# Performance work log

Measured on AMD Instinct MI355X. Metric: run time of the kernel, lower is better.

## Reference

```python
import jax, jax.numpy as jnp
import numpy as np

NEG_SLOPE = 0.2  # PyG GATv2Conv default

N_NODES = 10000
N_EDGES = 320000
DIM_IN = 128
DIM_H = 32
HEADS = 8
DIM_OUT = 32
HID = DIM_H * HEADS  # 256


def _gatv2(x, src, dst, Wl, Wr, att, bias, heads, ch, n):
    # x: [N, Fin]; src/dst: [E] (self-loops already included)
    xl = (x @ Wl).reshape(n, heads, ch)  # source-side transform
    xr = (x @ Wr).reshape(n, heads, ch)  # target-side transform
    e = jax.nn.leaky_relu(xl[src] + xr[dst], NEG_SLOPE)       # [E, H, C]
    score = jnp.einsum('ehc,hc->eh', e, att)                  # [E, H]
    m = jax.ops.segment_max(score, dst, num_segments=n)        # [N, H]
    ex = jnp.exp(score - m[dst])
    denom = jax.ops.segment_sum(ex, dst, num_segments=n)
    alpha = ex / (denom[dst] + 1e-16)                          # [E, H]
    out = jax.ops.segment_sum(alpha[:, :, None] * xl[src], dst, num_segments=n)
    return out.reshape(n, heads * ch) + bias


def setup_inputs() -> dict:
    key = jax.random.key(0)
    ks = jax.random.split(key, 16)
    x = jax.random.normal(ks[0], (N_NODES, DIM_IN), dtype=jnp.float32)
    edge_index = jax.random.randint(ks[1], (2, N_EDGES), 0, N_NODES, dtype=jnp.int64)

    def glorot(k, shape, fan_in):
        return jax.random.normal(k, shape, dtype=jnp.float32) * (1.0 / np.sqrt(fan_in))

    return {
        'x': x,
        'W1l': glorot(ks[2], (DIM_IN, HID), DIM_IN),
        'W1r': glorot(ks[3], (DIM_IN, HID), DIM_IN),
        'a1': glorot(ks[4], (HEADS, DIM_H), DIM_H),
        'b1': jnp.zeros((HID,), dtype=jnp.float32),
        'W2l': glorot(ks[5], (HID, HID), HID),
        'W2r': glorot(ks[6], (HID, HID), HID),
        'a2': glorot(ks[7], (HEADS, DIM_H), DIM_H),
        'b2': jnp.zeros((HID,), dtype=jnp.float32),
        'W3l': glorot(ks[8], (HID, DIM_OUT), HID),
        'W3r': glorot(ks[9], (HID, DIM_OUT), HID),
        'a3': glorot(ks[10], (1, DIM_OUT), DIM_OUT),
        'b3': jnp.zeros((DIM_OUT,), dtype=jnp.float32),
        'edge_index': edge_index,
    }


def reference(x, W1l, W1r, a1, b1, W2l, W2r, a2, b2, W3l, W3r, a3, b3, edge_index):
    n = x.shape[0]
    loops = jnp.arange(n, dtype=edge_index.dtype)
    src = jnp.concatenate([edge_index[0], loops])
    dst = jnp.concatenate([edge_index[1], loops])

    # eval mode: dropout(p=0.6) is identity
    h = _gatv2(x, src, dst, W1l, W1r, a1, b1, HEADS, DIM_H, n)
    h = jax.nn.relu(h)
    h_res = h
    h = _gatv2(h, src, dst, W2l, W2r, a2, b2, HEADS, DIM_H, n)
    h = h + h_res
    h = _gatv2(h, src, dst, W3l, W3r, a3, b3, 1, DIM_OUT, n)
    return h
```

## Files before the change

### kernel.cpp

```cpp
#include <hip/hip_runtime.h>

#define N_NODES 10000
#define N_EDGES 320000
#define E_TOT   (N_EDGES + N_NODES)
#define HID 256
#define NEG_SLOPE 0.2f
#define SLOTS 192

typedef __attribute__((ext_vector_type(8))) short short8;
typedef __attribute__((ext_vector_type(4))) float float4v;

__device__ int   g_cnt[N_NODES];
__device__ int   g_csr[(size_t)N_NODES * SLOTS];
__device__ __align__(16) float g_xl[(size_t)N_NODES * HID];
__device__ __align__(16) float g_xr[(size_t)N_NODES * HID];
__device__ __align__(16) float g_h1[(size_t)N_NODES * HID];
__device__ __align__(16) unsigned short g_xlb[(size_t)N_NODES * HID];
__device__ __align__(16) unsigned short g_abf[(size_t)N_NODES * 512];
__device__ __align__(16) unsigned short g_bp1a[16 * 8  * 64 * 8];
__device__ __align__(16) unsigned short g_bp2a[16 * 8  * 64 * 8];
__device__ __align__(16) unsigned short g_bp1b[16 * 16 * 64 * 8];
__device__ __align__(16) unsigned short g_bp2b[16 * 16 * 64 * 8];
__device__ __align__(16) unsigned short g_bp1c[2  * 16 * 64 * 8];
__device__ __align__(16) unsigned short g_bp2c[2  * 16 * 64 * 8];

__device__ __forceinline__ unsigned short f2bf(float f) {
    unsigned int u = __float_as_uint(f);
    unsigned int r = (u + 0x7fffu + ((u >> 16) & 1u)) >> 16;
    return (unsigned short)r;
}
__device__ __forceinline__ float bf2f(unsigned short h) {
    return __uint_as_float(((unsigned int)h) << 16);
}
__device__ __forceinline__ unsigned int splitpack(float f) {
    unsigned short hi = f2bf(f);
    unsigned short lo = f2bf(f - bf2f(hi));
    return ((unsigned int)lo << 16) | hi;
}

__device__ __forceinline__ void packB(const float* __restrict__ B,
                                      unsigned short* __restrict__ Bp,
                                      int t, int nkc, int N) {
    int lane = t & 63;
    int kc   = (t >> 6) % nkc;
    int nt   = (t >> 6) / nkc;
    int n = nt * 16 + (lane & 15);
    int kbase = kc * 32 + (lane >> 4) * 8;
    #pragma unroll
    for (int j = 0; j < 8; ++j) {
        int kp = kbase + j;
        int k  = kp >> 1;
        float f = B[(size_t)k * N + n];
        unsigned short hi = f2bf(f);
        Bp[(size_t)t * 8 + j] = (kp & 1) ? f2bf(f - bf2f(hi)) : hi;
    }
}

__global__ __launch_bounds__(256) void k_prep(const float* __restrict__ W1l,
                                              const float* __restrict__ W1r,
                                              const float* __restrict__ W2l,
                                              const float* __restrict__ W2r,
                                              const float* __restrict__ W3l,
                                              const float* __restrict__ W3r,
                                              unsigned short* bp1a, unsigned short* bp2a,
                                              unsigned short* bp1b, unsigned short* bp2b,
                                              unsigned short* bp1c, unsigned short* bp2c,
                                              int* __restrict__ cnt) {
    const int S0 = 16 * 8 * 64;
    const int S1 = 16 * 16 * 64;
    const int S2 = 2 * 16 * 64;
    int t = blockIdx.x * blockDim.x + threadIdx.x;
    if (t < S0) {
        packB(W1l, bp1a, t, 8, 256);
        packB(W1r, bp2a, t, 8, 256);
    } else if (t < S0 + S1) {
        int u = t - S0;
        packB(W2l, bp1b, u, 16, 256);
        packB(W2r, bp2b, u, 16, 256);
    } else if (t < S0 + S1 + S2) {
        int u = t - S0 - S1;
        packB(W3l, bp1c, u, 16, 32);
        packB(W3r, bp2c, u, 16, 32);
    } else {
        int u = t - S0 - S1 - S2;
        if (u < N_NODES) cnt[u] = 0;
    }
}

#define FILL_BLOCKS ((E_TOT + 255) / 256)
__global__ __launch_bounds__(256) void k_fill_gemm1(
    const int* __restrict__ ei,
    int* __restrict__ cnt, int* __restrict__ csr,
    const float4* __restrict__ A4,
    const short8* __restrict__ Bp1, const short8* __restrict__ Bp2,
    unsigned short* __restrict__ C1b,
    float* __restrict__ C2)
{
    if (blockIdx.x < FILL_BLOCKS) {
        int e = blockIdx.x * 256 + threadIdx.x;
        if (e < E_TOT) {
            int src, dst;
            if (e < N_EDGES) { src = ei[e]; dst = ei[N_EDGES + e]; }
            else             { src = dst = e - N_EDGES; }
            int pos = atomicAdd(&cnt[dst], 1);
            if (pos < SLOTS) csr[dst * SLOTS + pos] = src;
        }
        return;
    }
    const int nkc = 8;
    int mt   = blockIdx.x - FILL_BLOCKS;
    int lane = threadIdx.x & 63;
    int wid  = threadIdx.x >> 6;
    int quad = lane >> 4;
    int col  = lane & 15;
    int r0 = mt * 32 + col;       if (r0 >= N_NODES) r0 = N_NODES - 1;
    int r1 = mt * 32 + 16 + col;  if (r1 >= N_NODES) r1 = N_NODES - 1;
    const float4* a0 = A4 + (size_t)r0 * 32 + quad;
    const float4* a1 = A4 + (size_t)r1 * 32 + quad;
    float4v acc[2][4][2];
    #pragma unroll
    for (int s = 0; s < 2; ++s)
        #pragma unroll
        for (int t = 0; t < 4; ++t) { acc[s][t][0] = (float4v)(0.f); acc[s][t][1] = (float4v)(0.f); }
    for (int kc = 0; kc < nkc; ++kc) {
        float4 v0 = a0[kc * 4];
        float4 v1 = a1[kc * 4];
        union { short8 s; unsigned int u[4]; } c0, c1;
        c0.u[0] = splitpack(v0.x); c0.u[1] = splitpack(v0.y);
        c0.u[2] = splitpack(v0.z); c0.u[3] = splitpack(v0.w);
        c1.u[0] = splitpack(v1.x); c1.u[1] = splitpack(v1.y);
        c1.u[2] = splitpack(v1.z); c1.u[3] = splitpack(v1.w);
        short8 A0 = c0.s, A1 = c1.s;
        #pragma unroll
        for (int t = 0; t < 4; ++t) {
            int nt = wid * 4 + t;
            size_t bi = ((size_t)(nt * nkc + kc)) * 64 + lane;
            short8 b1 = Bp1[bi];
            short8 b2 = Bp2[bi];
            acc[0][t][0] = __builtin_amdgcn_mfma_f32_16x16x32_bf16(A0, b1, acc[0][t][0], 0, 0, 0);
            acc[0][t][1] = __builtin_amdgcn_mfma_f32_16x16x32_bf16(A0, b2, acc[0][t][1], 0, 0, 0);
            acc[1][t][0] = __builtin_amdgcn_mfma_f32_16x16x32_bf16(A1, b1, acc[1][t][0], 0, 0, 0);
            acc[1][t][1] = __builtin_amdgcn_mfma_f32_16x16x32_bf16(A1, b2, acc[1][t][1], 0, 0, 0);
        }
    }
    #pragma unroll
    for (int s = 0; s < 2; ++s) {
        #pragma unroll
        for (int t = 0; t < 4; ++t) {
            int gc = (wid * 4 + t) * 16 + col;
            #pragma unroll
            for (int r = 0; r < 4; ++r) {
                int row = mt * 32 + s * 16 + quad * 4 + r;
                if (row < N_NODES) {
                    C1b[(size_t)row * 256 + gc] = f2bf(acc[s][t][0][r]);
                    C2[(size_t)row * 256 + gc]  = acc[s][t][1][r];
                }
            }
        }
    }
}

__global__ __launch_bounds__(256) void k_mgemm2(const short8* __restrict__ Af,
                                                const short8* __restrict__ Bp1,
                                                const short8* __restrict__ Bp2,
                                                unsigned short* __restrict__ C1b,
                                                float* __restrict__ C2,
                                                int Kp, int nkc) {
    int mt   = blockIdx.x;
    int lane = threadIdx.x & 63;
    int wid  = threadIdx.x >> 6;
    int quad = lane >> 4;
    int col  = lane & 15;
    int ks   = Kp >> 3;
    int r0 = mt * 32 + col;       if (r0 >= N_NODES) r0 = N_NODES - 1;
    int r1 = mt * 32 + 16 + col;  if (r1 >= N_NODES) r1 = N_NODES - 1;
    const short8* a0 = Af + (size_t)r0 * ks + quad;
    const short8* a1 = Af + (size_t)r1 * ks + quad;
    float4v acc[2][4][2];
    #pragma unroll
    for (int s = 0; s < 2; ++s)
        #pragma unroll
        for (int t = 0; t < 4; ++t) { acc[s][t][0] = (float4v)(0.f); acc[s][t][1] = (float4v)(0.f); }
    for (int kc = 0; kc < nkc; ++kc) {
        short8 A0 = a0[kc * 4];
        short8 A1 = a1[kc * 4];
        #pragma unroll
        for (int t = 0; t < 4; ++t) {
            int nt = wid * 4 + t;
            size_t bi = ((size_t)(nt * nkc + kc)) * 64 + lane;
            short8 b1 = Bp1[bi];
            short8 b2 = Bp2[bi];
            acc[0][t][0] = __builtin_amdgcn_mfma_f32_16x16x32_bf16(A0, b1, acc[0][t][0], 0, 0, 0);
            acc[0][t][1] = __builtin_amdgcn_mfma_f32_16x16x32_bf16(A0, b2, acc[0][t][1], 0, 0, 0);
            acc[1][t][0] = __builtin_amdgcn_mfma_f32_16x16x32_bf16(A1, b1, acc[1][t][0], 0, 0, 0);
            acc[1][t][1] = __builtin_amdgcn_mfma_f32_16x16x32_bf16(A1, b2, acc[1][t][1], 0, 0, 0);
        }
    }
    #pragma unroll
    for (int s = 0; s < 2; ++s) {
        #pragma unroll
        for (int t = 0; t < 4; ++t) {
            int gc = (wid * 4 + t) * 16 + col;
            #pragma unroll
            for (int r = 0; r < 4; ++r) {
                int row = mt * 32 + s * 16 + quad * 4 + r;
                if (row < N_NODES) {
                    C1b[(size_t)row * 256 + gc] = f2bf(acc[s][t][0][r]);
                    C2[(size_t)row * 256 + gc]  = acc[s][t][1][r];
                }
            }
        }
    }
}

__global__ __launch_bounds__(256) void k_mgemm32(const short8* __restrict__ Af,
                                                 const short8* __restrict__ Bp1,
                                                 const short8* __restrict__ Bp2,
                                                 float* __restrict__ C1,
                                                 float* __restrict__ C2) {
    const int nkc = 16;
    int mt   = blockIdx.x;
    int lane = threadIdx.x & 63;
    int wid  = threadIdx.x >> 6;
    int quad = lane >> 4;
    int col  = lane & 15;
    int nt   = wid & 1;
    const short8* Bp = (wid < 2) ? Bp1 : Bp2;
    float* C = (wid < 2) ? C1 : C2;

    const short8* abase = Af + (size_t)(mt * 16 + col) * 64 + quad;
    float4v acc = (float4v)(0.f);
    #pragma unroll 4
    for (int kc = 0; kc < 16; ++kc) {
        short8 a = abase[kc * 4];
        short8 b = Bp[((size_t)(nt * 16 + kc)) * 64 + lane];
        acc = __builtin_amdgcn_mfma_f32_16x16x32_bf16(a, b, acc, 0, 0, 0);
    }
    #pragma unroll
    for (int r = 0; r < 4; ++r)
        C[(size_t)(mt * 16 + quad * 4 + r) * 32 + nt * 16 + col] = acc[r];
}

__global__ __launch_bounds__(256) void k_agg8(const unsigned short* __restrict__ xlb,
                                              const float4* __restrict__ xr4,
                                              const float4* __restrict__ att4,
                                              const float4* __restrict__ bias4,
                                              const int* __restrict__ cnt,
                                              const int* __restrict__ csr_src,
                                              const float4* __restrict__ res4,
                                              float4* __restrict__ out4,
                                              uint4* __restrict__ abf_out,
                                              int mode) {
    __shared__ float  ss[4][64];
    __shared__ float4 sacc[4][64];
    int node = blockIdx.x;
    int lane = threadIdx.x & 63;
    int wid  = threadIdx.x >> 6;
    float4 xrv = xr4[(size_t)node * 64 + lane];
    float4 av  = att4[lane];
    int c = cnt[node]; if (c > SLOTS) c = SLOTS;
    int start = node * SLOTS, end = start + c;

    float s = 0.f;
    float4 acc = make_float4(0.f, 0.f, 0.f, 0.f);

    for (int i0 = start + wid; i0 < end; i0 += 16) {
        ushort4 uv[4];
        #pragma unroll
        for (int j = 0; j < 4; ++j) {
            int e = i0 + 4 * j;
            int ec = e < end ? e : end - 1;
            int src = csr_src[ec];
            uv[j] = *(const ushort4*)(xlb + (size_t)src * 256 + 4 * lane);
        }
        #pragma unroll
        for (int j = 0; j < 4; ++j) {
            int e = i0 + 4 * j;
            if (e < end) {
                float4 xv;
                xv.x = bf2f(uv[j].x); xv.y = bf2f(uv[j].y);
                xv.z = bf2f(uv[j].z); xv.w = bf2f(uv[j].w);
                float tx = xv.x + xrv.x, ty = xv.y + xrv.y;
                float tz = xv.z + xrv.z, tw = xv.w + xrv.w;
                float w = (tx > 0.f ? tx : NEG_SLOPE * tx) * av.x
                        + (ty > 0.f ? ty : NEG_SLOPE * ty) * av.y
                        + (tz > 0.f ? tz : NEG_SLOPE * tz) * av.z
                        + (tw > 0.f ? tw : NEG_SLOPE * tw) * av.w;
                w += __shfl_xor(w, 1);
                w += __shfl_xor(w, 2);
                w += __shfl_xor(w, 4);
                float p = __expf(w);
                s += p;
                acc.x += p * xv.x;
                acc.y += p * xv.y;
                acc.z += p * xv.z;
                acc.w += p * xv.w;
            }
        }
    }
    ss[wid][lane] = s;
    sacc[wid][lane] = acc;
    __syncthreads();
    if (wid == 0) {
        float S = ss[0][lane] + ss[1][lane] + ss[2][lane] + ss[3][lane];
        float4 A = make_float4(0.f, 0.f, 0.f, 0.f);
        #pragma unroll
        for (int w = 0; w < 4; ++w) {
            float4 a = sacc[w][lane];
            A.x += a.x; A.y += a.y; A.z += a.z; A.w += a.w;
        }
        float inv = 1.f / (S + 1e-16f);
        float4 bv = bias4[lane];
        float4 o;
        o.x = A.x * inv + bv.x; o.y = A.y * inv + bv.y;
        o.z = A.z * inv + bv.z; o.w = A.w * inv + bv.w;
        if (mode == 0) {
            o.x = fmaxf(o.x, 0.f); o.y = fmaxf(o.y, 0.f);
            o.z = fmaxf(o.z, 0.f); o.w = fmaxf(o.w, 0.f);
        } else {
            float4 r = res4[(size_t)node * 64 + lane];
            o.x += r.x; o.y += r.y; o.z += r.z; o.w += r.w;
        }
        if (out4) out4[(size_t)node * 64 + lane] = o;
        if (abf_out) {
            uint4 u;
            u.x = splitpack(o.x); u.y = splitpack(o.y);
            u.z = splitpack(o.z); u.w = splitpack(o.w);
            abf_out[(size_t)node * 64 + lane] = u;
        }
    }
}

__global__ __launch_bounds__(256) void k_agg1(const float4* __restrict__ xl4,
                                              const float4* __restrict__ xr4,
                                              const float4* __restrict__ att4,
                                              const float4* __restrict__ bias4,
                                              const int* __restrict__ cnt,
                                              const int* __restrict__ csr_src,
                                              float4* __restrict__ out4) {
    int node = blockIdx.x * 4 + (threadIdx.x >> 6);
    if (node >= N_NODES) return;
    int lane = threadIdx.x & 63;
    int q = lane & 7;
    int grp = lane >> 3;
    float4 xrv = xr4[(size_t)node * 8 + q];
    float4 av  = att4[q];
    int c = cnt[node]; if (c > SLOTS) c = SLOTS;
    int start = node * SLOTS, end = start + c;
    float s = 0.f;
    float4 acc = make_float4(0.f, 0.f, 0.f, 0.f);
    for (int i = start + grp; i < end; i += 8) {
        int src = csr_src[i];
        float4 xv = xl4[(size_t)src * 8 + q];
        float tx = xv.x + xrv.x, ty = xv.y + xrv.y;
        float tz = xv.z + xrv.z, tw = xv.w + xrv.w;
        float w = (tx > 0.f ? tx : NEG_SLOPE * tx) * av.x
                + (ty > 0.f ? ty : NEG_SLOPE * ty) * av.y
                + (tz > 0.f ? tz : NEG_SLOPE * tz) * av.z
                + (tw > 0.f ? tw : NEG_SLOPE * tw) * av.w;
        w += __shfl_xor(w, 1);
        w += __shfl_xor(w, 2);
        w += __shfl_xor(w, 4);
        float p = __expf(w);
        s += p;
        acc.x += p * xv.x;
        acc.y += p * xv.y;
        acc.z += p * xv.z;
        acc.w += p * xv.w;
    }
    #pragma unroll
    for (int off = 8; off < 64; off <<= 1) {
        s     += __shfl_xor(s, off);
        acc.x += __shfl_xor(acc.x, off);
        acc.y += __shfl_xor(acc.y, off);
        acc.z += __shfl_xor(acc.z, off);
        acc.w += __shfl_xor(acc.w, off);
    }
    if (grp == 0) {
        float inv = 1.f / (s + 1e-16f);
        float4 bv = bias4[q];
        float4 o;
        o.x = acc.x * inv + bv.x; o.y = acc.y * inv + bv.y;
        o.z = acc.z * inv + bv.z; o.w = acc.w * inv + bv.w;
        out4[(size_t)node * 8 + q] = o;
    }
}


extern "C" void kernel_launch(void* const* d_in, const int* in_sizes, int n_in,
                              void* d_out, int out_size, void* d_ws, size_t ws_size,
                              hipStream_t stream) {
    const float* x   = (const float*)d_in[0];
    const float* W1l = (const float*)d_in[1];
    const float* W1r = (const float*)d_in[2];
    const float* a1  = (const float*)d_in[3];
    const float* b1  = (const float*)d_in[4];
    const float* W2l = (const float*)d_in[5];
    const float* W2r = (const float*)d_in[6];
    const float* a2  = (const float*)d_in[7];
    const float* b2  = (const float*)d_in[8];
    const float* W3l = (const float*)d_in[9];
    const float* W3r = (const float*)d_in[10];
    const float* a3  = (const float*)d_in[11];
    const float* b3  = (const float*)d_in[12];
    const int*   ei  = (const int*)d_in[13];
    float* out = (float*)d_out;

    int *cnt, *csr;
    float *xl, *xr, *h1;
    unsigned short *xlb, *abf, *bp1a, *bp2a, *bp1b, *bp2b, *bp1c, *bp2c;
    hipGetSymbolAddress((void**)&cnt,    HIP_SYMBOL(g_cnt));
    hipGetSymbolAddress((void**)&csr,    HIP_SYMBOL(g_csr));
    hipGetSymbolAddress((void**)&xl,     HIP_SYMBOL(g_xl));
    hipGetSymbolAddress((void**)&xr,     HIP_SYMBOL(g_xr));
    hipGetSymbolAddress((void**)&h1,     HIP_SYMBOL(g_h1));
    hipGetSymbolAddress((void**)&xlb,    HIP_SYMBOL(g_xlb));
    hipGetSymbolAddress((void**)&abf,    HIP_SYMBOL(g_abf));
    hipGetSymbolAddress((void**)&bp1a,   HIP_SYMBOL(g_bp1a));
    hipGetSymbolAddress((void**)&bp2a,   HIP_SYMBOL(g_bp2a));
    hipGetSymbolAddress((void**)&bp1b,   HIP_SYMBOL(g_bp1b));
    hipGetSymbolAddress((void**)&bp2b,   HIP_SYMBOL(g_bp2b));
    hipGetSymbolAddress((void**)&bp1c,   HIP_SYMBOL(g_bp1c));
    hipGetSymbolAddress((void**)&bp2c,   HIP_SYMBOL(g_bp2c));

    k_prep<<<144, 256, 0, stream>>>(W1l, W1r, W2l, W2r, W3l, W3r,
                                    bp1a, bp2a, bp1b, bp2b, bp1c, bp2c, cnt);

    k_fill_gemm1<<<FILL_BLOCKS + (N_NODES + 31) / 32, 256, 0, stream>>>(
        ei, cnt, csr, (const float4*)x,
        (const short8*)bp1a, (const short8*)bp2a, xlb, xr);

    k_agg8<<<N_NODES, 256, 0, stream>>>(xlb, (const float4*)xr,
                                        (const float4*)a1, (const float4*)b1,
                                        cnt, csr, nullptr, (float4*)h1,
                                        (uint4*)abf, 0);

    k_mgemm2<<<(N_NODES + 31) / 32, 256, 0, stream>>>((const short8*)abf,
                                                      (const short8*)bp1b, (const short8*)bp2b,
                                                      xlb, xr, 512, 16);

    k_agg8<<<N_NODES, 256, 0, stream>>>(xlb, (const float4*)xr,
                                        (const float4*)a2, (const float4*)b2,
                                        cnt, csr, (const float4*)h1, nullptr,
                                        (uint4*)abf, 1);

    k_mgemm32<<<N_NODES / 16, 256, 0, stream>>>((const short8*)abf,
                                                (const short8*)bp1c, (const short8*)bp2c,
                                                xl, xr);

    k_agg1<<<(N_NODES + 3) / 4, 256, 0, stream>>>((const float4*)xl, (const float4*)xr,
                                                  (const float4*)a3, (const float4*)b3,
                                                  cnt, csr, (float4*)out);
}
```

Measured before the change: 237.1 us.

## Fuse prep/fill/GEMM1 and layer-3 GEMM/aggregation into persistent kernels with grid barriers

Merges weight packing, counter clearing, CSR fill and the first GEMM into one persistent kernel, with an atomic grid-wide barrier between packing and the rest. It likewise merges the layer-3 GEMM and the single-head aggregation into one persistent kernel separated by a grid barrier. Each kernel resets the other's barrier counters so repeated calls work. The aim is to remove two kernel launches and their inter-kernel gaps. In exchange it relies on every block being co-resident for the spin barriers, or the kernels deadlock. The CSR fill now runs on far fewer blocks, each looping over edges.

```diff
diff --git a/kernel.cpp b/kernel.cpp
--- a/kernel.cpp
+++ b/kernel.cpp
@@ -7,9 +7,17 @@
 #define NEG_SLOPE 0.2f
 #define SLOTS 192
 
+#define PRE_BLOCKS   448
+#define GEMM1_TILES  ((N_NODES + 31) / 32)
+#define TAIL_BLOCKS  896
+#define L3_TILES     (N_NODES / 16)
+#define AGG1_GROUPS  ((N_NODES + 3) / 4)
+
 typedef __attribute__((ext_vector_type(8))) short short8;
 typedef __attribute__((ext_vector_type(4))) float float4v;
 
+__device__ int   g_barA[2];
+__device__ int   g_barB[2];
 __device__ int   g_cnt[N_NODES];
 __device__ int   g_csr[(size_t)N_NODES * SLOTS];
 __device__ __align__(16) float g_xl[(size_t)N_NODES * HID];
@@ -36,6 +44,21 @@
     unsigned short hi = f2bf(f);
     unsigned short lo = f2bf(f - bf2f(hi));
     return ((unsigned int)lo << 16) | hi;
+}
+
+__device__ __forceinline__ void gbar(int* bar, int nblk) {
+    __syncthreads();
+    if (threadIdx.x == 0) {
+        __threadfence();
+        if (atomicAdd(&bar[0], 1) + 1 == nblk) {
+            atomicExch(&bar[1], 1);
+        } else {
+            while (atomicAdd(&bar[1], 0) == 0)
+                __builtin_amdgcn_s_sleep(8);
+        }
+        __threadfence();
+    }
+    __syncthreads();
 }
 
 __device__ __forceinline__ void packB(const float* __restrict__ B,
@@ -56,49 +79,42 @@
     }
 }
 
-__global__ __launch_bounds__(256) void k_prep(const float* __restrict__ W1l,
-                                              const float* __restrict__ W1r,
-                                              const float* __restrict__ W2l,
-                                              const float* __restrict__ W2r,
-                                              const float* __restrict__ W3l,
-                                              const float* __restrict__ W3r,
-                                              unsigned short* bp1a, unsigned short* bp2a,
-                                              unsigned short* bp1b, unsigned short* bp2b,
-                                              unsigned short* bp1c, unsigned short* bp2c,
-                                              int* __restrict__ cnt) {
+__global__ __launch_bounds__(256, 2) void k_pre(
+    const float* __restrict__ W1l, const float* __restrict__ W1r,
+    const float* __restrict__ W2l, const float* __restrict__ W2r,
+    const float* __restrict__ W3l, const float* __restrict__ W3r,
+    int* __restrict__ cnt, const int* __restrict__ ei, int* __restrict__ csr,
+    const float4* __restrict__ A4,
+    unsigned short* __restrict__ C1b,
+    float* __restrict__ C2)
+{
     const int S0 = 16 * 8 * 64;
     const int S1 = 16 * 16 * 64;
     const int S2 = 2 * 16 * 64;
-    int t = blockIdx.x * blockDim.x + threadIdx.x;
-    if (t < S0) {
-        packB(W1l, bp1a, t, 8, 256);
-        packB(W1r, bp2a, t, 8, 256);
-    } else if (t < S0 + S1) {
-        int u = t - S0;
-        packB(W2l, bp1b, u, 16, 256);
-        packB(W2r, bp2b, u, 16, 256);
-    } else if (t < S0 + S1 + S2) {
-        int u = t - S0 - S1;
-        packB(W3l, bp1c, u, 16, 32);
-        packB(W3r, bp2c, u, 16, 32);
-    } else {
-        int u = t - S0 - S1 - S2;
-        if (u < N_NODES) cnt[u] = 0;
-    }
-}
-
-#define FILL_BLOCKS ((E_TOT + 255) / 256)
-__global__ __launch_bounds__(256) void k_fill_gemm1(
-    const int* __restrict__ ei,
-    int* __restrict__ cnt, int* __restrict__ csr,
-    const float4* __restrict__ A4,
-    const short8* __restrict__ Bp1, const short8* __restrict__ Bp2,
-    unsigned short* __restrict__ C1b,
-    float* __restrict__ C2)
-{
-    if (blockIdx.x < FILL_BLOCKS) {
-        int e = blockIdx.x * 256 + threadIdx.x;
-        if (e < E_TOT) {
+    int gtid = blockIdx.x * 256 + threadIdx.x;
+
+    if (gtid == 0) { g_barB[0] = 0; g_barB[1] = 0; }
+    for (int t = gtid; t < S0 + S1 + S2 + N_NODES; t += PRE_BLOCKS * 256) {
+        if (t < S0) {
+            packB(W1l, g_bp1a, t, 8, 256);
+            packB(W1r, g_bp2a, t, 8, 256);
+        } else if (t < S0 + S1) {
+            int u = t - S0;
+            packB(W2l, g_bp1b, u, 16, 256);
+            packB(W2r, g_bp2b, u, 16, 256);
+        } else if (t < S0 + S1 + S2) {
+            int u = t - S0 - S1;
+            packB(W3l, g_bp1c, u, 16, 32);
+            packB(W3r, g_bp2c, u, 16, 32);
+        } else {
+            cnt[t - S0 - S1 - S2] = 0;
+        }
+    }
+    gbar(g_barA, PRE_BLOCKS);
+
+    if (blockIdx.x >= GEMM1_TILES) {
+        for (int e = (blockIdx.x - GEMM1_TILES) * 256 + threadIdx.x;
+             e < E_TOT; e += (PRE_BLOCKS - GEMM1_TILES) * 256) {
             int src, dst;
             if (e < N_EDGES) { src = ei[e]; dst = ei[N_EDGES + e]; }
             else             { src = dst = e - N_EDGES; }
@@ -108,7 +124,7 @@
         return;
     }
     const int nkc = 8;
-    int mt   = blockIdx.x - FILL_BLOCKS;
+    int mt   = blockIdx.x;
     int lane = threadIdx.x & 63;
     int wid  = threadIdx.x >> 6;
     int quad = lane >> 4;
@@ -117,6 +133,8 @@
     int r1 = mt * 32 + 16 + col;  if (r1 >= N_NODES) r1 = N_NODES - 1;
     const float4* a0 = A4 + (size_t)r0 * 32 + quad;
     const float4* a1 = A4 + (size_t)r1 * 32 + quad;
+    const short8* Bp1 = (const short8*)g_bp1a;
+    const short8* Bp2 = (const short8*)g_bp2a;
     float4v acc[2][4][2];
     #pragma unroll
     for (int s = 0; s < 2; ++s)
@@ -211,34 +229,6 @@
             }
         }
     }
-}
-
-__global__ __launch_bounds__(256) void k_mgemm32(const short8* __restrict__ Af,
-                                                 const short8* __restrict__ Bp1,
-                                                 const short8* __restrict__ Bp2,
-                                                 float* __restrict__ C1,
-                                                 float* __restrict__ C2) {
-    const int nkc = 16;
-    int mt   = blockIdx.x;
-    int lane = threadIdx.x & 63;
-    int wid  = threadIdx.x >> 6;
-    int quad = lane >> 4;
-    int col  = lane & 15;
-    int nt   = wid & 1;
-    const short8* Bp = (wid < 2) ? Bp1 : Bp2;
-    float* C = (wid < 2) ? C1 : C2;
-
-    const short8* abase = Af + (size_t)(mt * 16 + col) * 64 + quad;
-    float4v acc = (float4v)(0.f);
-    #pragma unroll 4
-    for (int kc = 0; kc < 16; ++kc) {
-        short8 a = abase[kc * 4];
-        short8 b = Bp[((size_t)(nt * 16 + kc)) * 64 + lane];
-        acc = __builtin_amdgcn_mfma_f32_16x16x32_bf16(a, b, acc, 0, 0, 0);
-    }
-    #pragma unroll
-    for (int r = 0; r < 4; ++r)
-        C[(size_t)(mt * 16 + quad * 4 + r) * 32 + nt * 16 + col] = acc[r];
 }
 
 __global__ __launch_bounds__(256) void k_agg8(const unsigned short* __restrict__ xlb,
@@ -331,58 +321,89 @@
     }
 }
 
-__global__ __launch_bounds__(256) void k_agg1(const float4* __restrict__ xl4,
-                                              const float4* __restrict__ xr4,
-                                              const float4* __restrict__ att4,
-                                              const float4* __restrict__ bias4,
-                                              const int* __restrict__ cnt,
-                                              const int* __restrict__ csr_src,
-                                              float4* __restrict__ out4) {
-    int node = blockIdx.x * 4 + (threadIdx.x >> 6);
-    if (node >= N_NODES) return;
+__global__ __launch_bounds__(256, 4) void k_tail(
+    const short8* __restrict__ Af,
+    const short8* __restrict__ Bp1, const short8* __restrict__ Bp2,
+    float* __restrict__ C1, float* __restrict__ C2,
+    const int* __restrict__ cnt, const int* __restrict__ csr_src,
+    const float4* __restrict__ att4, const float4* __restrict__ bias4,
+    float4* __restrict__ out4)
+{
     int lane = threadIdx.x & 63;
-    int q = lane & 7;
-    int grp = lane >> 3;
-    float4 xrv = xr4[(size_t)node * 8 + q];
-    float4 av  = att4[q];
-    int c = cnt[node]; if (c > SLOTS) c = SLOTS;
-    int start = node * SLOTS, end = start + c;
-    float s = 0.f;
-    float4 acc = make_float4(0.f, 0.f, 0.f, 0.f);
-    for (int i = start + grp; i < end; i += 8) {
-        int src = csr_src[i];
-        float4 xv = xl4[(size_t)src * 8 + q];
-        float tx = xv.x + xrv.x, ty = xv.y + xrv.y;
-        float tz = xv.z + xrv.z, tw = xv.w + xrv.w;
-        float w = (tx > 0.f ? tx : NEG_SLOPE * tx) * av.x
-                + (ty > 0.f ? ty : NEG_SLOPE * ty) * av.y
-                + (tz > 0.f ? tz : NEG_SLOPE * tz) * av.z
-                + (tw > 0.f ? tw : NEG_SLOPE * tw) * av.w;
-        w += __shfl_xor(w, 1);
-        w += __shfl_xor(w, 2);
-        w += __shfl_xor(w, 4);
-        float p = __expf(w);
-        s += p;
-        acc.x += p * xv.x;
-        acc.y += p * xv.y;
-        acc.z += p * xv.z;
-        acc.w += p * xv.w;
-    }
-    #pragma unroll
-    for (int off = 8; off < 64; off <<= 1) {
-        s     += __shfl_xor(s, off);
-        acc.x += __shfl_xor(acc.x, off);
-        acc.y += __shfl_xor(acc.y, off);
-        acc.z += __shfl_xor(acc.z, off);
-        acc.w += __shfl_xor(acc.w, off);
-    }
-    if (grp == 0) {
-        float inv = 1.f / (s + 1e-16f);
-        float4 bv = bias4[q];
-        float4 o;
-        o.x = acc.x * inv + bv.x; o.y = acc.y * inv + bv.y;
-        o.z = acc.z * inv + bv.z; o.w = acc.w * inv + bv.w;
-        out4[(size_t)node * 8 + q] = o;
+    int wid  = threadIdx.x >> 6;
+    int quad = lane >> 4;
+    int col  = lane & 15;
+
+    if (blockIdx.x == 0 && threadIdx.x == 0) { g_barA[0] = 0; g_barA[1] = 0; }
+    {
+        int nt = wid & 1;
+        const short8* Bp = (wid < 2) ? Bp1 : Bp2;
+        float* C = (wid < 2) ? C1 : C2;
+        for (int mt = blockIdx.x; mt < L3_TILES; mt += TAIL_BLOCKS) {
+            const short8* abase = Af + (size_t)(mt * 16 + col) * 64 + quad;
+            float4v acc = (float4v)(0.f);
+            #pragma unroll 4
+            for (int kc = 0; kc < 16; ++kc) {
+                short8 a = abase[kc * 4];
+                short8 b = Bp[((size_t)(nt * 16 + kc)) * 64 + lane];
+                acc = __builtin_amdgcn_mfma_f32_16x16x32_bf16(a, b, acc, 0, 0, 0);
+            }
+            #pragma unroll
+            for (int r = 0; r < 4; ++r)
+                C[(size_t)(mt * 16 + quad * 4 + r) * 32 + nt * 16 + col] = acc[r];
+        }
+    }
+    gbar(g_barB, TAIL_BLOCKS);
+
+    {
+        const float4* xl4 = (const float4*)C1;
+        const float4* xr4 = (const float4*)C2;
+        int q = lane & 7;
+        int grp = lane >> 3;
+        for (int b = blockIdx.x; b < AGG1_GROUPS; b += TAIL_BLOCKS) {
+            int node = b * 4 + wid;
+            float4 xrv = xr4[(size_t)node * 8 + q];
+            float4 av  = att4[q];
+            int c = cnt[node]; if (c > SLOTS) c = SLOTS;
+            int start = node * SLOTS, end = start + c;
+            float s = 0.f;
+            float4 acc = make_float4(0.f, 0.f, 0.f, 0.f);
+            for (int i = start + grp; i < end; i += 8) {
+                int src = csr_src[i];
+                float4 xv = xl4[(size_t)src * 8 + q];
+                float tx = xv.x + xrv.x, ty = xv.y + xrv.y;
+                float tz = xv.z + xrv.z, tw = xv.w + xrv.w;
+                float w = (tx > 0.f ? tx : NEG_SLOPE * tx) * av.x
+                        + (ty > 0.f ? ty : NEG_SLOPE * ty) * av.y
+                        + (tz > 0.f ? tz : NEG_SLOPE * tz) * av.z
+                        + (tw > 0.f ? tw : NEG_SLOPE * tw) * av.w;
+                w += __shfl_xor(w, 1);
+                w += __shfl_xor(w, 2);
+                w += __shfl_xor(w, 4);
+                float p = __expf(w);
+                s += p;
+                acc.x += p * xv.x;
+                acc.y += p * xv.y;
+                acc.z += p * xv.z;
+                acc.w += p * xv.w;
+            }
+            #pragma unroll
+            for (int off = 8; off < 64; off <<= 1) {
+                s     += __shfl_xor(s, off);
+                acc.x += __shfl_xor(acc.x, off);
+                acc.y += __shfl_xor(acc.y, off);
+                acc.z += __shfl_xor(acc.z, off);
+                acc.w += __shfl_xor(acc.w, off);
+            }
+            if (grp == 0) {
+                float inv = 1.f / (s + 1e-16f);
+                float4 bv = bias4[q];
+                float4 o;
+                o.x = acc.x * inv + bv.x; o.y = acc.y * inv + bv.y;
+                o.z = acc.z * inv + bv.z; o.w = acc.w * inv + bv.w;
+                out4[(size_t)node * 8 + q] = o;
+            }
+        }
     }
 }
 
@@ -408,7 +429,7 @@
 
     int *cnt, *csr;
     float *xl, *xr, *h1;
-    unsigned short *xlb, *abf, *bp1a, *bp2a, *bp1b, *bp2b, *bp1c, *bp2c;
+    unsigned short *xlb, *abf, *bp1b, *bp2b, *bp1c, *bp2c;
     hipGetSymbolAddress((void**)&cnt,    HIP_SYMBOL(g_cnt));
     hipGetSymbolAddress((void**)&csr,    HIP_SYMBOL(g_csr));
     hipGetSymbolAddress((void**)&xl,     HIP_SYMBOL(g_xl));
@@ -416,19 +437,14 @@
     hipGetSymbolAddress((void**)&h1,     HIP_SYMBOL(g_h1));
     hipGetSymbolAddress((void**)&xlb,    HIP_SYMBOL(g_xlb));
     hipGetSymbolAddress((void**)&abf,    HIP_SYMBOL(g_abf));
-    hipGetSymbolAddress((void**)&bp1a,   HIP_SYMBOL(g_bp1a));
-    hipGetSymbolAddress((void**)&bp2a,   HIP_SYMBOL(g_bp2a));
     hipGetSymbolAddress((void**)&bp1b,   HIP_SYMBOL(g_bp1b));
     hipGetSymbolAddress((void**)&bp2b,   HIP_SYMBOL(g_bp2b));
     hipGetSymbolAddress((void**)&bp1c,   HIP_SYMBOL(g_bp1c));
     hipGetSymbolAddress((void**)&bp2c,   HIP_SYMBOL(g_bp2c));
 
-    k_prep<<<144, 256, 0, stream>>>(W1l, W1r, W2l, W2r, W3l, W3r,
-                                    bp1a, bp2a, bp1b, bp2b, bp1c, bp2c, cnt);
-
-    k_fill_gemm1<<<FILL_BLOCKS + (N_NODES + 31) / 32, 256, 0, stream>>>(
-        ei, cnt, csr, (const float4*)x,
-        (const short8*)bp1a, (const short8*)bp2a, xlb, xr);
+    k_pre<<<PRE_BLOCKS, 256, 0, stream>>>(W1l, W1r, W2l, W2r, W3l, W3r,
+                                          cnt, ei, csr,
+                                          (const float4*)x, xlb, xr);
 
     k_agg8<<<N_NODES, 256, 0, stream>>>(xlb, (const float4*)xr,
                                         (const float4*)a1, (const float4*)b1,
@@ -444,11 +460,9 @@
                                         cnt, csr, (const float4*)h1, nullptr,
                                         (uint4*)abf, 1);
 
-    k_mgemm32<<<N_NODES / 16, 256, 0, stream>>>((const short8*)abf,
-                                                (const short8*)bp1c, (const short8*)bp2c,
-                                                xl, xr);
-
-    k_agg1<<<(N_NODES + 3) / 4, 256, 0, stream>>>((const float4*)xl, (const float4*)xr,
-                                                  (const float4*)a3, (const float4*)b3,
-                                                  cnt, csr, (float4*)out);
-}
+    k_tail<<<TAIL_BLOCKS, 256, 0, stream>>>((const short8*)abf,
+                                            (const short8*)bp1c, (const short8*)bp2c,
+                                            xl, xr, cnt, csr,
+                                            (const float4*)a3, (const float4*)b3,
+                                            (float4*)out);
+}
```

Measured after the change: 363.3 us. 53.2% more time.

## Split bf16 xl into two half-channel planes and aggregate per half

Applied to the files above, without the earlier changes.

Stores the bf16 source features as two separate planes of 128 channels each and launches the 8-head aggregation with twice as many blocks, each handling one half of the channels (four heads) for a node. Each wave now processes two edges at once with 32 lanes per edge, so each gathered row is half as wide. The aim is a smaller gather working set per plane for better cache hit rates, plus more parallelism. The cost is that CSR indices are read twice and the xr, att and softmax work is split across two blocks. Some unused prep-kernel pointer arguments are also removed.

```diff
diff --git a/kernel.cpp b/kernel.cpp
--- a/kernel.cpp
+++ b/kernel.cpp
@@ -15,7 +15,7 @@
 __device__ __align__(16) float g_xl[(size_t)N_NODES * HID];
 __device__ __align__(16) float g_xr[(size_t)N_NODES * HID];
 __device__ __align__(16) float g_h1[(size_t)N_NODES * HID];
-__device__ __align__(16) unsigned short g_xlb[(size_t)N_NODES * HID];
+__device__ __align__(16) unsigned short g_xlb[2][(size_t)N_NODES * 128];
 __device__ __align__(16) unsigned short g_abf[(size_t)N_NODES * 512];
 __device__ __align__(16) unsigned short g_bp1a[16 * 8  * 64 * 8];
 __device__ __align__(16) unsigned short g_bp2a[16 * 8  * 64 * 8];
@@ -36,6 +36,12 @@
     unsigned short hi = f2bf(f);
     unsigned short lo = f2bf(f - bf2f(hi));
     return ((unsigned int)lo << 16) | hi;
+}
+
+__device__ __forceinline__ void store_xlb(unsigned short* xlb, int row, int gc,
+                                          float v) {
+    int half = gc >> 7;
+    xlb[(size_t)half * N_NODES * 128 + (size_t)row * 128 + (gc & 127)] = f2bf(v);
 }
 
 __device__ __forceinline__ void packB(const float* __restrict__ B,
@@ -62,25 +68,22 @@
                                               const float* __restrict__ W2r,
                                               const float* __restrict__ W3l,
                                               const float* __restrict__ W3r,
-                                              unsigned short* bp1a, unsigned short* bp2a,
-                                              unsigned short* bp1b, unsigned short* bp2b,
-                                              unsigned short* bp1c, unsigned short* bp2c,
                                               int* __restrict__ cnt) {
     const int S0 = 16 * 8 * 64;
     const int S1 = 16 * 16 * 64;
     const int S2 = 2 * 16 * 64;
     int t = blockIdx.x * blockDim.x + threadIdx.x;
     if (t < S0) {
-        packB(W1l, bp1a, t, 8, 256);
-        packB(W1r, bp2a, t, 8, 256);
+        packB(W1l, g_bp1a, t, 8, 256);
+        packB(W1r, g_bp2a, t, 8, 256);
     } else if (t < S0 + S1) {
         int u = t - S0;
-        packB(W2l, bp1b, u, 16, 256);
-        packB(W2r, bp2b, u, 16, 256);
+        packB(W2l, g_bp1b, u, 16, 256);
+        packB(W2r, g_bp2b, u, 16, 256);
     } else if (t < S0 + S1 + S2) {
         int u = t - S0 - S1;
-        packB(W3l, bp1c, u, 16, 32);
-        packB(W3r, bp2c, u, 16, 32);
+        packB(W3l, g_bp1c, u, 16, 32);
+        packB(W3r, g_bp2c, u, 16, 32);
     } else {
         int u = t - S0 - S1 - S2;
         if (u < N_NODES) cnt[u] = 0;
@@ -152,8 +155,8 @@
             for (int r = 0; r < 4; ++r) {
                 int row = mt * 32 + s * 16 + quad * 4 + r;
                 if (row < N_NODES) {
-                    C1b[(size_t)row * 256 + gc] = f2bf(acc[s][t][0][r]);
-                    C2[(size_t)row * 256 + gc]  = acc[s][t][1][r];
+                    store_xlb(C1b, row, gc, acc[s][t][0][r]);
+                    C2[(size_t)row * 256 + gc] = acc[s][t][1][r];
                 }
             }
         }
@@ -205,8 +208,8 @@
             for (int r = 0; r < 4; ++r) {
                 int row = mt * 32 + s * 16 + quad * 4 + r;
                 if (row < N_NODES) {
-                    C1b[(size_t)row * 256 + gc] = f2bf(acc[s][t][0][r]);
-                    C2[(size_t)row * 256 + gc]  = acc[s][t][1][r];
+                    store_xlb(C1b, row, gc, acc[s][t][0][r]);
+                    C2[(size_t)row * 256 + gc] = acc[s][t][1][r];
                 }
             }
         }
@@ -218,7 +221,6 @@
                                                  const short8* __restrict__ Bp2,
                                                  float* __restrict__ C1,
                                                  float* __restrict__ C2) {
-    const int nkc = 16;
     int mt   = blockIdx.x;
     int lane = threadIdx.x & 63;
     int wid  = threadIdx.x >> 6;
@@ -251,31 +253,39 @@
                                               float4* __restrict__ out4,
                                               uint4* __restrict__ abf_out,
                                               int mode) {
-    __shared__ float  ss[4][64];
-    __shared__ float4 sacc[4][64];
-    int node = blockIdx.x;
+    __shared__ float  ss[8][32];
+    __shared__ float4 sacc[8][32];
+    int bid  = blockIdx.x;
+    int half = (bid >= N_NODES) ? 1 : 0;
+    int node = bid - half * N_NODES;
     int lane = threadIdx.x & 63;
     int wid  = threadIdx.x >> 6;
-    float4 xrv = xr4[(size_t)node * 64 + lane];
-    float4 av  = att4[lane];
+    int sub  = lane >> 5;
+    int sl   = lane & 31;
+    int es   = wid * 2 + sub;
+    int cbase = half * 32 + sl;
+
+    const unsigned short* plane = xlb + (size_t)half * N_NODES * 128;
+    float4 xrv = xr4[(size_t)node * 64 + cbase];
+    float4 av  = att4[cbase];
     int c = cnt[node]; if (c > SLOTS) c = SLOTS;
     int start = node * SLOTS, end = start + c;
 
     float s = 0.f;
     float4 acc = make_float4(0.f, 0.f, 0.f, 0.f);
 
-    for (int i0 = start + wid; i0 < end; i0 += 16) {
+    for (int i0 = start + es; i0 < end; i0 += 32) {
         ushort4 uv[4];
         #pragma unroll
         for (int j = 0; j < 4; ++j) {
-            int e = i0 + 4 * j;
+            int e = i0 + 8 * j;
             int ec = e < end ? e : end - 1;
             int src = csr_src[ec];
-            uv[j] = *(const ushort4*)(xlb + (size_t)src * 256 + 4 * lane);
+            uv[j] = *(const ushort4*)(plane + (size_t)src * 128 + 4 * sl);
         }
         #pragma unroll
         for (int j = 0; j < 4; ++j) {
-            int e = i0 + 4 * j;
+            int e = i0 + 8 * j;
             if (e < end) {
                 float4 xv;
                 xv.x = bf2f(uv[j].x); xv.y = bf2f(uv[j].y);
@@ -298,19 +308,21 @@
             }
         }
     }
-    ss[wid][lane] = s;
-    sacc[wid][lane] = acc;
+    ss[es][sl] = s;
+    sacc[es][sl] = acc;
     __syncthreads();
-    if (wid == 0) {
-        float S = ss[0][lane] + ss[1][lane] + ss[2][lane] + ss[3][lane];
+    if (threadIdx.x < 32) {
+        int q = threadIdx.x;
+        float S = 0.f;
         float4 A = make_float4(0.f, 0.f, 0.f, 0.f);
         #pragma unroll
-        for (int w = 0; w < 4; ++w) {
-            float4 a = sacc[w][lane];
+        for (int k = 0; k < 8; ++k) {
+            S += ss[k][q];
+            float4 a = sacc[k][q];
             A.x += a.x; A.y += a.y; A.z += a.z; A.w += a.w;
         }
         float inv = 1.f / (S + 1e-16f);
-        float4 bv = bias4[lane];
+        float4 bv = bias4[half * 32 + q];
         float4 o;
         o.x = A.x * inv + bv.x; o.y = A.y * inv + bv.y;
         o.z = A.z * inv + bv.z; o.w = A.w * inv + bv.w;
@@ -318,15 +330,15 @@
             o.x = fmaxf(o.x, 0.f); o.y = fmaxf(o.y, 0.f);
             o.z = fmaxf(o.z, 0.f); o.w = fmaxf(o.w, 0.f);
         } else {
-            float4 r = res4[(size_t)node * 64 + lane];
+            float4 r = res4[(size_t)node * 64 + half * 32 + q];
             o.x += r.x; o.y += r.y; o.z += r.z; o.w += r.w;
         }
-        if (out4) out4[(size_t)node * 64 + lane] = o;
+        if (out4) out4[(size_t)node * 64 + half * 32 + q] = o;
         if (abf_out) {
             uint4 u;
             u.x = splitpack(o.x); u.y = splitpack(o.y);
             u.z = splitpack(o.z); u.w = splitpack(o.w);
-            abf_out[(size_t)node * 64 + lane] = u;
+            abf_out[(size_t)node * 64 + half * 32 + q] = u;
         }
     }
 }
@@ -423,26 +435,25 @@
     hipGetSymbolAddress((void**)&bp1c,   HIP_SYMBOL(g_bp1c));
     hipGetSymbolAddress((void**)&bp2c,   HIP_SYMBOL(g_bp2c));
 
-    k_prep<<<144, 256, 0, stream>>>(W1l, W1r, W2l, W2r, W3l, W3r,
-                                    bp1a, bp2a, bp1b, bp2b, bp1c, bp2c, cnt);
+    k_prep<<<144, 256, 0, stream>>>(W1l, W1r, W2l, W2r, W3l, W3r, cnt);
 
     k_fill_gemm1<<<FILL_BLOCKS + (N_NODES + 31) / 32, 256, 0, stream>>>(
         ei, cnt, csr, (const float4*)x,
         (const short8*)bp1a, (const short8*)bp2a, xlb, xr);
 
-    k_agg8<<<N_NODES, 256, 0, stream>>>(xlb, (const float4*)xr,
-                                        (const float4*)a1, (const float4*)b1,
-                                        cnt, csr, nullptr, (float4*)h1,
-                                        (uint4*)abf, 0);
+    k_agg8<<<2 * N_NODES, 256, 0, stream>>>(xlb, (const float4*)xr,
+                                            (const float4*)a1, (const float4*)b1,
+                                            cnt, csr, nullptr, (float4*)h1,
+                                            (uint4*)abf, 0);
 
     k_mgemm2<<<(N_NODES + 31) / 32, 256, 0, stream>>>((const short8*)abf,
                                                       (const short8*)bp1b, (const short8*)bp2b,
                                                       xlb, xr, 512, 16);
 
-    k_agg8<<<N_NODES, 256, 0, stream>>>(xlb, (const float4*)xr,
-                                        (const float4*)a2, (const float4*)b2,
-                                        cnt, csr, (const float4*)h1, nullptr,
-                                        (uint4*)abf, 1);
+    k_agg8<<<2 * N_NODES, 256, 0, stream>>>(xlb, (const float4*)xr,
+                                            (const float4*)a2, (const float4*)b2,
+                                            cnt, csr, (const float4*)h1, nullptr,
+                                            (uint4*)abf, 1);
 
     k_mgemm32<<<N_NODES / 16, 256, 0, stream>>>((const short8*)abf,
                                                 (const short8*)bp1c, (const short8*)bp2c,
```

Measured after the change: 244.4 us. 1.03x slower.
